# Optimization experiments

Hardware: AMD Instinct MI355X
Metric: run time of the kernel (lower is better)

The kernel has to match this reference:

```python
import jax, jax.numpy as jnp
import numpy as np

B, S, D = 4, 2048, 512
H, Dh = 8, 64  # head_dim(=num heads)=8, qkv_dim(per-head)=64
SCALE = 1.0 / float(np.sqrt(Dh))


def setup_inputs() -> dict:
    key = jax.random.key(0)
    ks = jax.random.split(key, 11)
    w = 1.0 / float(np.sqrt(D))
    return {
        "x": jax.random.normal(ks[0], (B, S, D), dtype=jnp.float32),
        "mask": jax.random.randint(ks[1], (B, 1, S, S), 0, 2, dtype=jnp.int32),
        "Wq": jax.random.normal(ks[2], (D, H * Dh), dtype=jnp.float32) * w,
        "bq": jax.random.normal(ks[3], (H * Dh,), dtype=jnp.float32) * w,
        "Wk": jax.random.normal(ks[4], (D, H * Dh), dtype=jnp.float32) * w,
        "bk": jax.random.normal(ks[5], (H * Dh,), dtype=jnp.float32) * w,
        "Wv": jax.random.normal(ks[6], (D, H * Dh), dtype=jnp.float32) * w,
        "bv": jax.random.normal(ks[7], (H * Dh,), dtype=jnp.float32) * w,
        "Wo": jax.random.normal(ks[8], (H * Dh, D), dtype=jnp.float32) * w,
        "bo": jax.random.normal(ks[9], (D,), dtype=jnp.float32) * w,
    }


def reference(x, mask, Wq, bq, Wk, bk, Wv, bv, Wo, bo):
    b = x.shape[0]
    q = (x @ Wq + bq).reshape(b, S, H, Dh)
    k = (x @ Wk + bk).reshape(b, S, H, Dh)
    v = (x @ Wv + bv).reshape(b, S, H, Dh)
    # [b,h,q,k] attention scores, softmax over k
    score = jax.nn.softmax(jnp.einsum('bqhd,bkhd->bhqk', q, k) * SCALE, axis=-1)
    # faithful quirk: mask applied AFTER softmax, masked entries set to 1e-20
    score = jnp.where(mask == 1, jnp.float32(1e-20), score)
    # faithful quirk: einsum 'bvhd,bhqk->bvhd' sums score over q AND k -> [b,h] scalar per head
    s = score.sum(axis=(-2, -1))  # [b, h]
    att = v * s[:, None, :, None]  # [b, S, H, Dh]
    out = att.reshape(b, S, H * Dh) @ Wo + bo
    return out
```

## Files before the change

### kernel.cpp

```cpp
#include <hip/hip_runtime.h>
#include <cstdint>
#include <cstddef>

#define DEVINL __device__ __forceinline__

constexpr int S_ = 2048;
constexpr int D_ = 512;
constexpr int H_ = 8;
constexpr float SCALE_ = 0.125f;
constexpr float SCALE_L2E_ = 0.18033688011112f;

using short8 = __attribute__((ext_vector_type(8))) short;
using f32x4  = __attribute__((ext_vector_type(4))) float;

DEVINL unsigned short f2bf(float f){
  unsigned u = __builtin_bit_cast(unsigned, f);
  u += 0x7FFFu + ((u >> 16) & 1u);
  return (unsigned short)(u >> 16);
}
DEVINL float bf2f(unsigned short h){
  return __builtin_bit_cast(float, ((unsigned)h) << 16);
}

DEVINL float fast_exp2(float x){ return __builtin_amdgcn_exp2f(x); }

DEVINL void gload16(const void* g, void* l){
  __builtin_amdgcn_global_load_lds(
      (__attribute__((address_space(1))) void*)(g),
      (__attribute__((address_space(3))) void*)(l), 16, 0, 0);
}

__global__ void cast_x_kernel(const float* __restrict__ x, unsigned short* __restrict__ xb){
  int i = blockIdx.x * 256 + threadIdx.x;
  const float* p = x + (size_t)i * 8;
  float4 a = *(const float4*)p;
  float4 b = *(const float4*)(p + 4);
  short8 o;
  o[0]=f2bf(a.x); o[1]=f2bf(a.y); o[2]=f2bf(a.z); o[3]=f2bf(a.w);
  o[4]=f2bf(b.x); o[5]=f2bf(b.y); o[6]=f2bf(b.z); o[7]=f2bf(b.w);
  *(short8*)(xb + (size_t)i*8) = o;
}

__global__ void mask_bits_kernel(const int* __restrict__ mask, unsigned char* __restrict__ bits){
  unsigned tid = blockIdx.x * 256 + threadIdx.x;
  #pragma unroll
  for (int it = 0; it < 4; ++it){
    size_t bidx = (size_t)tid + (size_t)it * 524288;
    const int* p = mask + bidx * 8;
    int4 a = *(const int4*)p;
    int4 c = *(const int4*)(p + 4);
    unsigned v = (unsigned)(a.x != 0)       | ((unsigned)(a.y != 0) << 1)
               | ((unsigned)(a.z != 0) << 2) | ((unsigned)(a.w != 0) << 3)
               | ((unsigned)(c.x != 0) << 4) | ((unsigned)(c.y != 0) << 5)
               | ((unsigned)(c.z != 0) << 6) | ((unsigned)(c.w != 0) << 7);
    bits[bidx] = (unsigned char)v;
  }
}

__global__ void castT_kernel(const float* __restrict__ W0, const float* __restrict__ W1,
                             const float* __restrict__ W2, const float* __restrict__ W3,
                             unsigned short* __restrict__ WT){
  __shared__ float tile[32][33];
  const int z = blockIdx.z;
  const float* W = (z==0) ? W0 : (z==1 ? W1 : (z==2 ? W2 : W3));
  const float scale = (z==0) ? SCALE_L2E_ : 1.0f;
  unsigned short* out = WT + (size_t)z * D_ * D_;
  int n0 = blockIdx.x*32, k0 = blockIdx.y*32;
  int tx = threadIdx.x, ty = threadIdx.y;
  #pragma unroll
  for (int j=0;j<4;j++)
    tile[ty+j*8][tx] = W[(size_t)(k0+ty+j*8)*D_ + n0+tx];
  __syncthreads();
  #pragma unroll
  for (int j=0;j<4;j++)
    out[(size_t)(n0+ty+j*8)*D_ + k0+tx] = f2bf(tile[tx][ty+j*8]*scale);
}

template<typename OutT>
__global__ __launch_bounds__(256) void gemm_bt(
    const unsigned short* __restrict__ A, long long Az,
    const unsigned short* __restrict__ BT, long long Bz,
    const float* __restrict__ bias0, const float* __restrict__ bias1, const float* __restrict__ bias2,
    float bs0, float bs1, float bs2,
    OutT* __restrict__ Cp, long long Cz)
{
  __shared__ unsigned short As[128*64];
  __shared__ unsigned short Bs[128*64];
  const int z = blockIdx.z;
  const unsigned short* Ab = A + (size_t)z*Az;
  const unsigned short* Bb = BT + (size_t)z*Bz;
  const float* bias = (z==0) ? bias0 : (z==1 ? bias1 : bias2);
  const float bscale = (z==0) ? bs0 : (z==1 ? bs1 : bs2);
  OutT* C = Cp + (size_t)z*Cz;
  const int m0 = blockIdx.y*128, n0 = blockIdx.x*128;
  const int t = threadIdx.x, lane = t & 63, w = t >> 6;
  const int wr = w >> 1, wc = w & 1;
  const int g = lane >> 4, lq = lane & 15;
  f32x4 acc[4][4] = {};
  for (int kk = 0; kk < D_; kk += 64){
    #pragma unroll
    for (int p = 0; p < 4; p++){
      int o = p*4096 + t*16;
      int row = o >> 7;
      int cb  = o & 127;
      int scb = cb ^ ((row & 7) << 4);
      gload16((const char*)Ab + ((size_t)(m0+row)*D_ + kk)*2 + scb, (char*)As + o);
      gload16((const char*)Bb + ((size_t)(n0+row)*D_ + kk)*2 + scb, (char*)Bs + o);
    }
    __syncthreads();
    #pragma unroll
    for (int ks = 0; ks < 2; ks++){
      short8 af[4], bf[4];
      #pragma unroll
      for (int i = 0; i < 4; i++){
        int rowA = wr*64 + i*16 + lq;
        af[i] = *(const short8*)((const char*)As + ((rowA*128 + ks*64 + g*16) ^ ((rowA&7)<<4)));
        int rowB = wc*64 + i*16 + lq;
        bf[i] = *(const short8*)((const char*)Bs + ((rowB*128 + ks*64 + g*16) ^ ((rowB&7)<<4)));
      }
      #pragma unroll
      for (int i = 0; i < 4; i++)
        #pragma unroll
        for (int j = 0; j < 4; j++)
          acc[i][j] = __builtin_amdgcn_mfma_f32_16x16x32_bf16(af[i], bf[j], acc[i][j], 0, 0, 0);
    }
    __syncthreads();
  }
  #pragma unroll
  for (int i = 0; i < 4; i++){
    #pragma unroll
    for (int j = 0; j < 4; j++){
      int col = n0 + wc*64 + j*16 + lq;
      float bvv = bias[col]*bscale;
      #pragma unroll
      for (int r = 0; r < 4; r++){
        int row = m0 + wr*64 + i*16 + g*4 + r;
        float v = acc[i][j][r] + bvv;
        if constexpr (sizeof(OutT) == 4) C[(size_t)row*D_ + col] = (OutT)v;
        else                             C[(size_t)row*D_ + col] = (OutT)f2bf(v);
      }
    }
  }
}

__global__ __launch_bounds__(512) void attn_zm_kernel(
    const unsigned short* __restrict__ Q, const unsigned short* __restrict__ Kg,
    const unsigned* __restrict__ bitsW, float* __restrict__ Zp, float* __restrict__ Mp)
{
  __shared__ unsigned short Ks[256*64];
  const int bid = blockIdx.x;
  const int kz = bid & 7;
  const int qt = (bid >> 3) & 3;
  const int bh = bid >> 5;
  const int b = bh >> 3, h = bh & 7;
  const int t = threadIdx.x, lane = t & 63, w = t >> 6;
  const int g = lane >> 4, lq = lane & 15;
  const int qbase = qt*512 + w*64;

  const char* Kgb = (const char*)Kg + ((size_t)(b*S_ + kz*256))*1024 + h*128;
  #pragma unroll
  for (int p = 0; p < 4; p++){
    int o = p*8192 + t*16;
    int row = o >> 7;
    int scb = (o & 127) ^ ((row & 7) << 4);
    gload16(Kgb + (size_t)row*1024 + scb, (char*)Ks + o);
  }

  unsigned wb[4][8];
  #pragma unroll
  for (int qs = 0; qs < 4; qs++){
    const uint4* wp = (const uint4*)(bitsW + ((size_t)(b*S_ + qbase + qs*16 + lq))*(S_/32) + kz*8);
    uint4 wA = wp[0], wB = wp[1];
    wb[qs][0]=wA.x; wb[qs][1]=wA.y; wb[qs][2]=wA.z; wb[qs][3]=wA.w;
    wb[qs][4]=wB.x; wb[qs][5]=wB.y; wb[qs][6]=wB.z; wb[qs][7]=wB.w;
  }

  short8 qf[4][2];
  #pragma unroll
  for (int qs = 0; qs < 4; qs++)
    #pragma unroll
    for (int c = 0; c < 2; c++)
      qf[qs][c] = *(const short8*)(Q + ((size_t)(b*S_ + qbase + qs*16 + lq))*D_ + h*64 + c*32 + g*8);

  float Z[4], Mm[4];
  #pragma unroll
  for (int qs = 0; qs < 4; qs++){ Z[qs] = 0.f; Mm[qs] = 0.f; }

  __syncthreads();

  #pragma unroll
  for (int i = 0; i < 16; ++i){
    const int kt2 = i >> 1, ks = i & 1;
    const int row = i*16 + lq;
    const int sw = (row & 7) << 4;
    short8 A0 = *(const short8*)((const char*)Ks + row*128 + ((g*16) ^ sw));
    short8 A1 = *(const short8*)((const char*)Ks + row*128 + ((64 + g*16) ^ sw));
    #pragma unroll
    for (int qs = 0; qs < 4; qs++){
      f32x4 d = {0.f,0.f,0.f,0.f};
      d = __builtin_amdgcn_mfma_f32_16x16x32_bf16(A0, qf[qs][0], d, 0, 0, 0);
      d = __builtin_amdgcn_mfma_f32_16x16x32_bf16(A1, qf[qs][1], d, 0, 0, 0);
      unsigned nib = wb[qs][kt2] >> (ks*16 + g*4);
      #pragma unroll
      for (int r = 0; r < 4; r++){
        float p = fast_exp2(d[r]);
        Z[qs] += p;
        Mm[qs] = fmaf((float)((nib >> r) & 1u), p, Mm[qs]);
      }
    }
  }
  #pragma unroll
  for (int qs = 0; qs < 4; qs++){
    Z[qs]  += __shfl_xor(Z[qs], 16);  Mm[qs] += __shfl_xor(Mm[qs], 16);
    Z[qs]  += __shfl_xor(Z[qs], 32);  Mm[qs] += __shfl_xor(Mm[qs], 32);
  }
  if (g == 0){
    size_t base = ((size_t)(kz*32 + bh))*S_ + qbase + lq;
    #pragma unroll
    for (int qs = 0; qs < 4; qs++){
      Zp[base + qs*16] = Z[qs];
      Mp[base + qs*16] = Mm[qs];
    }
  }
}

__global__ __launch_bounds__(256) void finalize_s(const float* __restrict__ Zp,
                                                  const float* __restrict__ Mp,
                                                  float* __restrict__ sbh){
  const int bh = blockIdx.x;
  const int t = threadIdx.x;
  float acc = 0.f;
  for (int q = t; q < S_; q += 256){
    float z = 0.f, m = 0.f;
    #pragma unroll
    for (int kz = 0; kz < 8; kz++){
      size_t idx = ((size_t)(kz*32 + bh))*S_ + q;
      z += Zp[idx];
      m += Mp[idx];
    }
    acc += (z - m) / z;
  }
  #pragma unroll
  for (int m = 1; m < 64; m <<= 1) acc += __shfl_xor(acc, m);
  __shared__ float wsum[4];
  if ((t & 63) == 0) wsum[t >> 6] = acc;
  __syncthreads();
  if (t == 0) sbh[bh] = wsum[0] + wsum[1] + wsum[2] + wsum[3];
}

__global__ void scale_woT_kernel(const unsigned short* __restrict__ WoT,
                                 const float* __restrict__ sbh,
                                 unsigned short* __restrict__ outw){
  int i = blockIdx.x*256 + threadIdx.x;
  size_t e = (size_t)i * 8;
  int k = (int)(e & 511);
  int n = (int)((e >> 9) & 511);
  int b = (int)(e >> 18);
  float sv = sbh[b*H_ + (k >> 6)];
  short8 wv = *(const short8*)(WoT + (size_t)n*D_ + k);
  short8 o;
  #pragma unroll
  for (int j = 0; j < 8; j++) o[j] = (short)f2bf(bf2f((unsigned short)wv[j]) * sv);
  *(short8*)(outw + e) = o;
}

extern "C" void kernel_launch(void* const* d_in, const int* in_sizes, int n_in,
                              void* d_out, int out_size, void* d_ws, size_t ws_size,
                              hipStream_t stream) {
  (void)in_sizes; (void)n_in; (void)out_size; (void)ws_size;
  const float* x  = (const float*)d_in[0];
  const int* mask = (const int*)d_in[1];
  const float* Wq = (const float*)d_in[2];
  const float* bq = (const float*)d_in[3];
  const float* Wk = (const float*)d_in[4];
  const float* bk = (const float*)d_in[5];
  const float* Wv = (const float*)d_in[6];
  const float* bv = (const float*)d_in[7];
  const float* Wo = (const float*)d_in[8];
  const float* bo = (const float*)d_in[9];
  float* out = (float*)d_out;

  char* ws = (char*)d_ws;
  unsigned short* xb   = (unsigned short*)(ws);
  unsigned short* wT   = (unsigned short*)(ws +  8388608);
  unsigned short* woT  = (unsigned short*)(ws +  9961472);
  unsigned short* Qb   = (unsigned short*)(ws + 10485760);
  unsigned short* Kb   = (unsigned short*)(ws + 18874368);
  unsigned short* Vb   = (unsigned short*)(ws + 27262976);
  unsigned short* woST = (unsigned short*)(ws + 35651584);
  float*          sbh  = (float*)         (ws + 37748736);
  float*          Zp   = (float*)(ws);
  float*          Mp   = (float*)(ws + 2097152);
  unsigned char*  bits = (unsigned char*)(ws + 35651584);

  cast_x_kernel<<<2048, 256, 0, stream>>>(x, xb);
  castT_kernel<<<dim3(16,16,4), dim3(32,8), 0, stream>>>(Wq, Wk, Wv, Wo, wT);
  mask_bits_kernel<<<2048, 256, 0, stream>>>(mask, bits);

  gemm_bt<unsigned short><<<dim3(4,64,3), 256, 0, stream>>>(
      xb, 0LL, wT, 262144LL, bq, bk, bv, SCALE_L2E_, 1.0f, 1.0f, Qb, 4194304LL);

  attn_zm_kernel<<<1024, 512, 0, stream>>>(Qb, Kb, (const unsigned*)bits, Zp, Mp);
  finalize_s<<<32, 256, 0, stream>>>(Zp, Mp, sbh);

  scale_woT_kernel<<<512, 256, 0, stream>>>(woT, sbh, woST);

  gemm_bt<float><<<dim3(4,16,4), 256, 0, stream>>>(
      Vb, 1048576LL, woST, 262144LL, bo, bo, bo, 1.0f, 1.0f, 1.0f, out, 1048576LL);
}
```

Baseline: 110.0 us.

## Merge prep kernels into one launch and split attention K load into two stages

The x cast, mask bit-packing and weight transpose/cast kernels are combined into a single prep kernel that branches on block index, removing two launches and the gaps between them. In the attention kernel the K tile load is split into two 128-row halves with separate vmcnt waits and barriers, so MFMA work on the first half can start while the second half is still loading. The mask-bit and Q loads are moved ahead of the K loads so the vmcnt accounting lines up. The prep kernel applies __syncthreads only in its transpose branch, and the explicit waitcnt counts depend on the exact number of global loads issued.

```diff
diff --git a/kernel.cpp b/kernel.cpp
--- a/kernel.cpp
+++ b/kernel.cpp
@@ -30,50 +30,54 @@
       (__attribute__((address_space(3))) void*)(l), 16, 0, 0);
 }
 
-__global__ void cast_x_kernel(const float* __restrict__ x, unsigned short* __restrict__ xb){
-  int i = blockIdx.x * 256 + threadIdx.x;
-  const float* p = x + (size_t)i * 8;
-  float4 a = *(const float4*)p;
-  float4 b = *(const float4*)(p + 4);
-  short8 o;
-  o[0]=f2bf(a.x); o[1]=f2bf(a.y); o[2]=f2bf(a.z); o[3]=f2bf(a.w);
-  o[4]=f2bf(b.x); o[5]=f2bf(b.y); o[6]=f2bf(b.z); o[7]=f2bf(b.w);
-  *(short8*)(xb + (size_t)i*8) = o;
-}
-
-__global__ void mask_bits_kernel(const int* __restrict__ mask, unsigned char* __restrict__ bits){
-  unsigned tid = blockIdx.x * 256 + threadIdx.x;
-  #pragma unroll
-  for (int it = 0; it < 4; ++it){
-    size_t bidx = (size_t)tid + (size_t)it * 524288;
-    const int* p = mask + bidx * 8;
-    int4 a = *(const int4*)p;
-    int4 c = *(const int4*)(p + 4);
-    unsigned v = (unsigned)(a.x != 0)       | ((unsigned)(a.y != 0) << 1)
-               | ((unsigned)(a.z != 0) << 2) | ((unsigned)(a.w != 0) << 3)
-               | ((unsigned)(c.x != 0) << 4) | ((unsigned)(c.y != 0) << 5)
-               | ((unsigned)(c.z != 0) << 6) | ((unsigned)(c.w != 0) << 7);
-    bits[bidx] = (unsigned char)v;
-  }
-}
-
-__global__ void castT_kernel(const float* __restrict__ W0, const float* __restrict__ W1,
-                             const float* __restrict__ W2, const float* __restrict__ W3,
-                             unsigned short* __restrict__ WT){
+__global__ __launch_bounds__(256) void prep_kernel(
+    const float* __restrict__ x, unsigned short* __restrict__ xb,
+    const int* __restrict__ mask, unsigned char* __restrict__ bits,
+    const float* __restrict__ W0, const float* __restrict__ W1,
+    const float* __restrict__ W2, const float* __restrict__ W3,
+    unsigned short* __restrict__ WT)
+{
   __shared__ float tile[32][33];
-  const int z = blockIdx.z;
-  const float* W = (z==0) ? W0 : (z==1 ? W1 : (z==2 ? W2 : W3));
-  const float scale = (z==0) ? SCALE_L2E_ : 1.0f;
-  unsigned short* out = WT + (size_t)z * D_ * D_;
-  int n0 = blockIdx.x*32, k0 = blockIdx.y*32;
-  int tx = threadIdx.x, ty = threadIdx.y;
-  #pragma unroll
-  for (int j=0;j<4;j++)
-    tile[ty+j*8][tx] = W[(size_t)(k0+ty+j*8)*D_ + n0+tx];
-  __syncthreads();
-  #pragma unroll
-  for (int j=0;j<4;j++)
-    out[(size_t)(n0+ty+j*8)*D_ + k0+tx] = f2bf(tile[tx][ty+j*8]*scale);
+  const int bid = blockIdx.x, t = threadIdx.x;
+  if (bid < 2048){
+    int i = bid * 256 + t;
+    const float* p = x + (size_t)i * 8;
+    float4 a = *(const float4*)p;
+    float4 b = *(const float4*)(p + 4);
+    short8 o;
+    o[0]=f2bf(a.x); o[1]=f2bf(a.y); o[2]=f2bf(a.z); o[3]=f2bf(a.w);
+    o[4]=f2bf(b.x); o[5]=f2bf(b.y); o[6]=f2bf(b.z); o[7]=f2bf(b.w);
+    *(short8*)(xb + (size_t)i*8) = o;
+  } else if (bid < 4096){
+    unsigned tid = (bid - 2048) * 256 + t;
+    #pragma unroll
+    for (int it = 0; it < 4; ++it){
+      size_t bidx = (size_t)tid + (size_t)it * 524288;
+      const int* p = mask + bidx * 8;
+      int4 a = *(const int4*)p;
+      int4 c = *(const int4*)(p + 4);
+      unsigned v = (unsigned)(a.x != 0)       | ((unsigned)(a.y != 0) << 1)
+                 | ((unsigned)(a.z != 0) << 2) | ((unsigned)(a.w != 0) << 3)
+                 | ((unsigned)(c.x != 0) << 4) | ((unsigned)(c.y != 0) << 5)
+                 | ((unsigned)(c.z != 0) << 6) | ((unsigned)(c.w != 0) << 7);
+      bits[bidx] = (unsigned char)v;
+    }
+  } else {
+    const int b2 = bid - 4096;
+    const int z = b2 >> 8, r = b2 & 255;
+    const float* W = (z==0) ? W0 : (z==1 ? W1 : (z==2 ? W2 : W3));
+    const float scale = (z==0) ? SCALE_L2E_ : 1.0f;
+    unsigned short* out = WT + (size_t)z * D_ * D_;
+    const int n0 = (r & 15)*32, k0 = (r >> 4)*32;
+    const int tx = t & 31, ty = t >> 5;
+    #pragma unroll
+    for (int j=0;j<4;j++)
+      tile[ty+j*8][tx] = W[(size_t)(k0+ty+j*8)*D_ + n0+tx];
+    __syncthreads();
+    #pragma unroll
+    for (int j=0;j<4;j++)
+      out[(size_t)(n0+ty+j*8)*D_ + k0+tx] = f2bf(tile[tx][ty+j*8]*scale);
+  }
 }
 
 template<typename OutT>
@@ -147,7 +151,7 @@
     const unsigned short* __restrict__ Q, const unsigned short* __restrict__ Kg,
     const unsigned* __restrict__ bitsW, float* __restrict__ Zp, float* __restrict__ Mp)
 {
-  __shared__ unsigned short Ks[256*64];
+  __shared__ unsigned short Ks[2][128*64];
   const int bid = blockIdx.x;
   const int kz = bid & 7;
   const int qt = (bid >> 3) & 3;
@@ -157,15 +161,6 @@
   const int g = lane >> 4, lq = lane & 15;
   const int qbase = qt*512 + w*64;
 
-  const char* Kgb = (const char*)Kg + ((size_t)(b*S_ + kz*256))*1024 + h*128;
-  #pragma unroll
-  for (int p = 0; p < 4; p++){
-    int o = p*8192 + t*16;
-    int row = o >> 7;
-    int scb = (o & 127) ^ ((row & 7) << 4);
-    gload16(Kgb + (size_t)row*1024 + scb, (char*)Ks + o);
-  }
-
   unsigned wb[4][8];
   #pragma unroll
   for (int qs = 0; qs < 4; qs++){
@@ -174,41 +169,69 @@
     wb[qs][0]=wA.x; wb[qs][1]=wA.y; wb[qs][2]=wA.z; wb[qs][3]=wA.w;
     wb[qs][4]=wB.x; wb[qs][5]=wB.y; wb[qs][6]=wB.z; wb[qs][7]=wB.w;
   }
-
   short8 qf[4][2];
   #pragma unroll
   for (int qs = 0; qs < 4; qs++)
     #pragma unroll
     for (int c = 0; c < 2; c++)
       qf[qs][c] = *(const short8*)(Q + ((size_t)(b*S_ + qbase + qs*16 + lq))*D_ + h*64 + c*32 + g*8);
+  __builtin_amdgcn_sched_barrier(0);
+
+  const char* Kgb = (const char*)Kg + ((size_t)(b*S_ + kz*256))*1024 + h*128;
+  #pragma unroll
+  for (int p = 0; p < 2; p++){
+    int o = p*8192 + t*16;
+    int row = o >> 7;
+    int scb = (o & 127) ^ ((row & 7) << 4);
+    gload16(Kgb + (size_t)row*1024 + scb, (char*)Ks[0] + o);
+  }
+  #pragma unroll
+  for (int p = 0; p < 2; p++){
+    int o = p*8192 + t*16;
+    int row = o >> 7;
+    int scb = (o & 127) ^ ((row & 7) << 4);
+    gload16(Kgb + (size_t)(row + 128)*1024 + scb, (char*)Ks[1] + o);
+  }
 
   float Z[4], Mm[4];
   #pragma unroll
   for (int qs = 0; qs < 4; qs++){ Z[qs] = 0.f; Mm[qs] = 0.f; }
 
-  __syncthreads();
-
-  #pragma unroll
-  for (int i = 0; i < 16; ++i){
-    const int kt2 = i >> 1, ks = i & 1;
-    const int row = i*16 + lq;
-    const int sw = (row & 7) << 4;
-    short8 A0 = *(const short8*)((const char*)Ks + row*128 + ((g*16) ^ sw));
-    short8 A1 = *(const short8*)((const char*)Ks + row*128 + ((64 + g*16) ^ sw));
-    #pragma unroll
-    for (int qs = 0; qs < 4; qs++){
-      f32x4 d = {0.f,0.f,0.f,0.f};
-      d = __builtin_amdgcn_mfma_f32_16x16x32_bf16(A0, qf[qs][0], d, 0, 0, 0);
-      d = __builtin_amdgcn_mfma_f32_16x16x32_bf16(A1, qf[qs][1], d, 0, 0, 0);
-      unsigned nib = wb[qs][kt2] >> (ks*16 + g*4);
-      #pragma unroll
-      for (int r = 0; r < 4; r++){
-        float p = fast_exp2(d[r]);
-        Z[qs] += p;
-        Mm[qs] = fmaf((float)((nib >> r) & 1u), p, Mm[qs]);
-      }
-    }
-  }
+  asm volatile("s_waitcnt vmcnt(2)" ::: "memory");
+  __builtin_amdgcn_sched_barrier(0);
+  __builtin_amdgcn_s_barrier();
+
+#define ATTN_HALF(HB, WOFF)                                                       \
+  _Pragma("unroll")                                                               \
+  for (int i = 0; i < 8; ++i){                                                    \
+    const int row = i*16 + lq;                                                    \
+    const int sw = (row & 7) << 4;                                                \
+    short8 A0 = *(const short8*)((const char*)Ks[HB] + row*128 + ((g*16) ^ sw));  \
+    short8 A1 = *(const short8*)((const char*)Ks[HB] + row*128 + ((64 + g*16) ^ sw)); \
+    _Pragma("unroll")                                                             \
+    for (int qs = 0; qs < 4; qs++){                                               \
+      f32x4 d = {0.f,0.f,0.f,0.f};                                                \
+      d = __builtin_amdgcn_mfma_f32_16x16x32_bf16(A0, qf[qs][0], d, 0, 0, 0);     \
+      d = __builtin_amdgcn_mfma_f32_16x16x32_bf16(A1, qf[qs][1], d, 0, 0, 0);     \
+      unsigned nib = wb[qs][WOFF + (i >> 1)] >> ((i & 1)*16 + g*4);               \
+      _Pragma("unroll")                                                           \
+      for (int r = 0; r < 4; r++){                                                \
+        float p = fast_exp2(d[r]);                                                \
+        Z[qs] += p;                                                               \
+        Mm[qs] = fmaf((float)((nib >> r) & 1u), p, Mm[qs]);                       \
+      }                                                                           \
+    }                                                                             \
+  }
+
+  ATTN_HALF(0, 0)
+
+  asm volatile("s_waitcnt vmcnt(0)" ::: "memory");
+  __builtin_amdgcn_sched_barrier(0);
+  __builtin_amdgcn_s_barrier();
+
+  ATTN_HALF(1, 4)
+#undef ATTN_HALF
+
   #pragma unroll
   for (int qs = 0; qs < 4; qs++){
     Z[qs]  += __shfl_xor(Z[qs], 16);  Mm[qs] += __shfl_xor(Mm[qs], 16);
@@ -293,9 +316,7 @@
   float*          Mp   = (float*)(ws + 2097152);
   unsigned char*  bits = (unsigned char*)(ws + 35651584);
 
-  cast_x_kernel<<<2048, 256, 0, stream>>>(x, xb);
-  castT_kernel<<<dim3(16,16,4), dim3(32,8), 0, stream>>>(Wq, Wk, Wv, Wo, wT);
-  mask_bits_kernel<<<2048, 256, 0, stream>>>(mask, bits);
+  prep_kernel<<<5120, 256, 0, stream>>>(x, xb, mask, bits, Wq, Wk, Wv, Wo, wT);
 
   gemm_bt<unsigned short><<<dim3(4,64,3), 256, 0, stream>>>(
       xb, 0LL, wT, 262144LL, bq, bk, bv, SCALE_L2E_, 1.0f, 1.0f, Qb, 4194304LL);
```

Result: faster. 102.8 us (-6.5%).
